# Kernel optimization log

Hardware: AMD Instinct MI355X
Metric: run time of the kernel (lower is better)

## Reference

```python
import jax, jax.numpy as jnp
import numpy as np

S = 32   # parent grid side
G = 64   # child grid side (2*S)
C = 16   # channels
DN = ('NDHWC', 'DHWIO', 'NDHWC')


def conv3(t, w, b):
    # t: [D,H,W,Cin] dense grid; zero padding == nonexistent coords contribute 0 (ME semantics)
    return jax.lax.conv_general_dilated(t[None], w, (1, 1, 1), 'SAME', dimension_numbers=DN)[0] + b


def _grids():
    ix = jnp.arange(G)
    px = (ix % 2)[:, None, None]
    py = (ix % 2)[None, :, None]
    pz = (ix % 2)[None, None, :]
    oct_m = {(a, b, c): (px == a) & (py == b) & (pz == c)
             for a in (0, 1) for b in (0, 1) for c in (0, 1)}
    groups6 = [[(0, 0, 0)], [(1, 1, 0)], [(1, 0, 1)], [(0, 1, 1)],
               [(1, 0, 0), (0, 1, 0)], [(0, 0, 1), (1, 1, 1)]]
    g6 = [jnp.any(jnp.stack([oct_m[o] for o in g]), 0) for g in groups6]
    s3 = (ix // 2)[:, None, None] + (ix // 2)[None, :, None] + (ix // 2)[None, None, :]
    m3 = [(s3 % 3) == j for j in range(3)]  # 3-way repartition (group_mask_gen_par)
    return g6, m3


def coder(feat, occ, w1, b1, w2, b2):
    # ProbCoder: conv -> ReLU -> conv -> sigmoid; outputs exist only at input coords
    of = occ[..., None].astype(feat.dtype)
    h = jax.nn.relu(conv3(feat, w1, b1)) * of
    return jax.nn.sigmoid(conv3(h, w2, b2)) * of


def union(a, b):
    (fa, oa), (fb, ob) = a, b
    return (jnp.where(oa[..., None], fa, fb), oa | ob)


def _forward(x, w_down, b_down, w_fel1, b_fel1, w_fel2, b_fel2, w_up, b_up,
             wc1, bc1, wc2, bc2, wl1, bl1, wl2, bl2):
    g6, m3 = _grids()
    occ_x = x[..., 0] > 0                                    # GT occupied child voxels
    # down (stride-2 conv): coordinate effect only -- last_POV uses ones_like features
    p_occ = jnp.any(occ_x.reshape(S, 2, S, 2, S, 2), axis=(1, 3, 5))  # parent coords
    pf = p_occ[..., None].astype(x.dtype)                    # last_POV features (ones)
    # FEL (dfa): conv(1->C,k3)+ReLU+conv(C->C,k3), outputs only at existing parents
    h = jax.nn.relu(conv3(pf, w_fel1, b_fel1)) * pf
    h = conv3(h, w_fel2, b_fel2) * pf                        # [S,S,S,C]
    # generative transposed conv k2 s2: each parent emits 8 children (octant-specific weight)
    up = jnp.einsum('xyzc,ocd->xyzod', h, w_up) + b_up       # [S,S,S,8,C]
    up = up.reshape(S, S, S, 2, 2, 2, C).transpose(0, 3, 1, 4, 2, 5, 6).reshape(G, G, G, C)
    occ = jnp.repeat(jnp.repeat(jnp.repeat(p_occ, 2, 0), 2, 1), 2, 2)  # child coords of prob
    prob_f = up * occ[..., None]
    lab = [occ_x & g for g in g6]                            # generate_label: GT per group
    # ---------- anchor1 compression (3 sub-stages inside octant group 1) ----------
    a1_o = occ & g6[0]
    a1_f = prob_f * a1_o[..., None]
    r = [(a1_f * m[..., None], a1_o & m) for m in m3]
    lab1 = [lab[0] & m for m in m3]
    p11 = coder(r[0][0], r[0][1], wc1[0], bc1[0], wc2[0], bc2[0])
    d1s = (prob_f * lab1[0][..., None], lab1[0])             # decoded GT of sub-stage 1
    in2 = union(r[1], d1s)
    p12 = coder(in2[0], in2[1], wl1[0], bl1[0], wl2[0], bl2[0]) * (in2[1] & m3[1])[..., None]
    d2s = (prob_f * lab1[1][..., None], lab1[1])
    in3 = union(union(d1s, d2s), r[2])
    p13 = coder(in3[0], in3[1], wl1[1], bl1[1], wl2[1], bl2[1]) * (in3[1] & m3[2])[..., None]
    # ---------- anchors 2..6 ----------
    dec = (prob_f * lab[0][..., None], lab[0])               # prob_anchor1_dec
    probs = [p11, p12, p13]
    for k in range(1, 6):
        ak_o = occ & g6[k]
        ak = (prob_f * ak_o[..., None], ak_o)
        inp = union(dec, ak)
        pk = coder(inp[0], inp[1], wc1[k], bc1[k], wc2[k], bc2[k]) * (inp[1] & g6[k])[..., None]
        probs.append(pk)
        if k < 5:
            dk = (prob_f * lab[k][..., None], lab[k])
            dec = union(dec, dk)
    probs = jnp.stack([p[..., 0] for p in probs], 0)          # [8,G,G,G]
    labels = jnp.stack([lab1[0], lab1[1], lab1[2], lab[1], lab[2], lab[3], lab[4], lab[5]], 0).astype(x.dtype)
    return probs, labels


def setup_inputs() -> dict:
    key = jax.random.key(0)
    ks = jax.random.split(key, 20)
    f = lambda k, s: jax.random.normal(k, s, jnp.float32) * 0.1
    x = (jax.random.uniform(ks[0], (G, G, G, 1)) < 0.5).astype(jnp.float32)
    return {
        'x': x,
        'w_down': f(ks[1], (2, 2, 2, 1, 1)), 'b_down': f(ks[2], (1,)),
        'w_fel1': f(ks[3], (3, 3, 3, 1, C)), 'b_fel1': f(ks[4], (C,)),
        'w_fel2': f(ks[5], (3, 3, 3, C, C)), 'b_fel2': f(ks[6], (C,)),
        'w_up': f(ks[7], (8, C, C)), 'b_up': f(ks[8], (C,)),
        'wc1': f(ks[9], (6, 3, 3, 3, C, C)), 'bc1': f(ks[10], (6, C)),
        'wc2': f(ks[11], (6, 3, 3, 3, C, 1)), 'bc2': f(ks[12], (6, 1)),
        'wl1': f(ks[13], (2, 5, 5, 5, C, C)), 'bl1': f(ks[14], (2, C)),
        'wl2': f(ks[15], (2, 5, 5, 5, C, 1)), 'bl2': f(ks[16], (2, 1)),
    }


def reference(x, w_down, b_down, w_fel1, b_fel1, w_fel2, b_fel2, w_up, b_up,
              wc1, bc1, wc2, bc2, wl1, bl1, wl2, bl2):
    return _forward(x, w_down, b_down, w_fel1, b_fel1, w_fel2, b_fel2, w_up, b_up,
                    wc1, bc1, wc2, bc2, wl1, bl1, wl2, bl2)
```

## Files before the change

kernel.cpp:

```cpp
#include <hip/hip_runtime.h>
#include <cstdint>
#include <math.h>

#define G 64
#define S 32
#define G3 (G*G*G)
#define S3 (S*S*S)

typedef unsigned long long u64;
typedef unsigned int u32;
typedef unsigned short u16;

typedef __attribute__((ext_vector_type(8))) short s16x8;
typedef __attribute__((ext_vector_type(4))) float f32x4;

__device__ __forceinline__ float sigmoidf_(float v) {
    return 1.0f / (1.0f + expf(-v));
}
__device__ __forceinline__ u32 f2bf_rne(float f) {
    u32 u = __float_as_uint(f);
    u += 0x7fff + ((u >> 16) & 1);
    return u >> 16;
}
__device__ __forceinline__ u64 rfl64(u64 v) {
    u32 lo = __builtin_amdgcn_readfirstlane((u32)v);
    u32 hi = __builtin_amdgcn_readfirstlane((u32)(v >> 32));
    return ((u64)hi << 32) | lo;
}
__device__ __forceinline__ u64 tap_hit(u64 wout, u64 wn, int dz) {
    return (dz >= 0) ? (wout & (wn >> dz)) : (wout & (wn << (-dz)));
}

__global__ __launch_bounds__(256) void k_pocc(const float* __restrict__ x,
                                              unsigned char* __restrict__ pocc) {
    int p = blockIdx.x * 256 + threadIdx.x;
    if (p >= S3) return;
    int pz = p & 31, py = (p >> 5) & 31, px = p >> 10;
    const float* b = x + (((size_t)(px * 2) * G + py * 2) * G + pz * 2);
    bool occ = false;
    #pragma unroll
    for (int a = 0; a < 2; a++)
        #pragma unroll
        for (int bb = 0; bb < 2; bb++)
            #pragma unroll
            for (int c = 0; c < 2; c++)
                occ = occ || (b[((size_t)a * G + bb) * G + c] > 0.0f);
    pocc[p] = occ ? 1 : 0;
}

__global__ __launch_bounds__(256) void k_fel1(const unsigned char* __restrict__ pocc,
                                              const float* __restrict__ w1,
                                              const float* __restrict__ b1,
                                              float* __restrict__ h1) {
    int p = blockIdx.x * 256 + threadIdx.x;
    if (p >= S3) return;
    int pz = p & 31, py = (p >> 5) & 31, px = p >> 10;
    float* o = h1 + (size_t)p * 16;
    if (!pocc[p]) {
        #pragma unroll
        for (int i = 0; i < 16; i++) o[i] = 0.0f;
        return;
    }
    float acc[16];
    #pragma unroll
    for (int i = 0; i < 16; i++) acc[i] = b1[i];
    for (int dx = -1; dx <= 1; ++dx) {
        int nx = px + dx; if ((unsigned)nx >= S) continue;
        for (int dy = -1; dy <= 1; ++dy) {
            int ny = py + dy; if ((unsigned)ny >= S) continue;
            for (int dz = -1; dz <= 1; ++dz) {
                int nz = pz + dz; if ((unsigned)nz >= S) continue;
                if (pocc[(nx * S + ny) * S + nz]) {
                    const float* w = w1 + (((dx + 1) * 3 + (dy + 1)) * 3 + (dz + 1)) * 16;
                    #pragma unroll
                    for (int i = 0; i < 16; i++) acc[i] += w[i];
                }
            }
        }
    }
    #pragma unroll
    for (int i = 0; i < 16; i++) o[i] = fmaxf(acc[i], 0.0f);
}

__global__ __launch_bounds__(256) void k_fel2(const unsigned char* __restrict__ pocc,
                                              const float* __restrict__ h1,
                                              const float* __restrict__ w2,
                                              const float* __restrict__ b2,
                                              float* __restrict__ h2) {
    int p = blockIdx.x * 256 + threadIdx.x;
    if (p >= S3) return;
    int pz = p & 31, py = (p >> 5) & 31, px = p >> 10;
    float* o = h2 + (size_t)p * 16;
    if (!pocc[p]) {
        #pragma unroll
        for (int i = 0; i < 16; i++) o[i] = 0.0f;
        return;
    }
    float acc[16];
    #pragma unroll
    for (int i = 0; i < 16; i++) acc[i] = b2[i];
    for (int dx = -1; dx <= 1; ++dx) {
        int nx = px + dx; if ((unsigned)nx >= S) continue;
        for (int dy = -1; dy <= 1; ++dy) {
            int ny = py + dy; if ((unsigned)ny >= S) continue;
            for (int dz = -1; dz <= 1; ++dz) {
                int nz = pz + dz; if ((unsigned)nz >= S) continue;
                const float* f = h1 + (size_t)((nx * S + ny) * S + nz) * 16;
                const float* w = w2 + (((dx + 1) * 3 + (dy + 1)) * 3 + (dz + 1)) * 256;
                #pragma unroll
                for (int ci = 0; ci < 16; ++ci) {
                    float fv = f[ci];
                    #pragma unroll
                    for (int co = 0; co < 16; ++co)
                        acc[co] = fmaf(fv, w[ci * 16 + co], acc[co]);
                }
            }
        }
    }
    #pragma unroll
    for (int i = 0; i < 16; i++) o[i] = acc[i];
}

__global__ __launch_bounds__(256) void k_up(const unsigned char* __restrict__ pocc,
                                            const float* __restrict__ h2,
                                            const float* __restrict__ wup,
                                            const float* __restrict__ bup,
                                            u16* __restrict__ probf16) {
    int p = blockIdx.x * 256 + threadIdx.x;
    if (p >= S3) return;
    int pz = p & 31, py = (p >> 5) & 31, px = p >> 10;
    bool occ = pocc[p] != 0;
    float h[16];
    const float* hp = h2 + (size_t)p * 16;
    #pragma unroll
    for (int i = 0; i < 16; i++) h[i] = hp[i];
    #pragma unroll
    for (int o = 0; o < 8; o++) {
        int a = o >> 2, b = (o >> 1) & 1, c = o & 1;
        u16* op = probf16 + (((size_t)(2 * px + a) * G + (2 * py + b)) * G + (2 * pz + c)) * 16;
        uint4* o4 = reinterpret_cast<uint4*>(op);
        if (!occ) {
            o4[0] = make_uint4(0, 0, 0, 0);
            o4[1] = make_uint4(0, 0, 0, 0);
        } else {
            u32 pk[8];
            #pragma unroll
            for (int i = 0; i < 8; ++i) {
                float a0 = bup[2 * i], a1 = bup[2 * i + 1];
                #pragma unroll
                for (int cc = 0; cc < 16; cc++) {
                    a0 = fmaf(h[cc], wup[(o * 16 + cc) * 16 + 2 * i], a0);
                    a1 = fmaf(h[cc], wup[(o * 16 + cc) * 16 + 2 * i + 1], a1);
                }
                pk[i] = f2bf_rne(a0) | (f2bf_rne(a1) << 16);
            }
            o4[0] = make_uint4(pk[0], pk[1], pk[2], pk[3]);
            o4[1] = make_uint4(pk[4], pk[5], pk[6], pk[7]);
        }
    }
}

__global__ __launch_bounds__(256) void k_masks(const float* __restrict__ x,
                                               const unsigned char* __restrict__ pocc,
                                               u64* __restrict__ lw_in,
                                               u64* __restrict__ lw_fin,
                                               float* __restrict__ labels) {
    int z = threadIdx.x;
    int y = blockIdx.x * 4 + threadIdx.y;
    int xx = blockIdx.y;
    int v = (xx * G + y) * G + z;
    int par = ((xx & 1) << 2) | ((y & 1) << 1) | (z & 1);
    const int gmap[8] = {0, 5, 4, 3, 4, 2, 1, 5};
    int g = gmap[par];
    int t = ((xx >> 1) + (y >> 1) + (z >> 1)) % 3;
    bool occ = pocc[(((xx >> 1) * S) + (y >> 1)) * S + (z >> 1)] != 0;
    bool ox = x[v] > 0.0f;
    bool g0 = (g == 0);

    bool mi[8], mf[8], lb[8];
    mi[0] = occ && g0 && (t == 0);
    mi[1] = (occ && g0 && (t == 1)) || (ox && g0 && (t == 0));
    mi[2] = (ox && g0 && (t < 2)) || (occ && g0 && (t == 2));
    mi[3] = (ox && g0)       || (occ && (g == 1));
    mi[4] = (ox && (g <= 1)) || (occ && (g == 2));
    mi[5] = (ox && (g <= 2)) || (occ && (g == 3));
    mi[6] = (ox && (g <= 3)) || (occ && (g == 4));
    mi[7] = (ox && (g <= 4)) || (occ && (g == 5));

    mf[0] = occ && g0 && (t == 0);
    mf[1] = occ && g0 && (t == 1);
    mf[2] = occ && g0 && (t == 2);
    mf[3] = occ && (g == 1);
    mf[4] = occ && (g == 2);
    mf[5] = occ && (g == 3);
    mf[6] = occ && (g == 4);
    mf[7] = occ && (g == 5);

    lb[0] = ox && g0 && (t == 0);
    lb[1] = ox && g0 && (t == 1);
    lb[2] = ox && g0 && (t == 2);
    lb[3] = ox && (g == 1);
    lb[4] = ox && (g == 2);
    lb[5] = ox && (g == 3);
    lb[6] = ox && (g == 4);
    lb[7] = ox && (g == 5);

    int line = xx * G + y;
    #pragma unroll
    for (int c = 0; c < 8; ++c) {
        u64 wi = __ballot((int)mi[c]);
        u64 wf = __ballot((int)mf[c]);
        if (z == 0) {
            lw_in[c * 4096 + line] = wi;
            lw_fin[c * 4096 + line] = wf;
        }
        labels[(size_t)c * G3 + v] = lb[c] ? 1.0f : 0.0f;
    }
}

#define FRAGSTRIDE 38400
__global__ __launch_bounds__(64) void k_prep_bfrag(const float* __restrict__ wc1,
                                                   const float* __restrict__ wl1,
                                                   u16* __restrict__ bfrag) {
    int c = blockIdx.x;
    int frag = blockIdx.y;
    int lane = threadIdx.x;
    bool is5 = (c == 1 || c == 2);
    int R = is5 ? 2 : 1;
    int KS = 2 * R + 1;
    int npair = R + 1;
    int nfrag = KS * KS * npair;
    if (frag >= nfrag) return;
    const float* W = is5 ? (wl1 + (size_t)(c - 1) * 32000)
                         : (wc1 + (size_t)((c == 0) ? 0 : (c - 2)) * 6912);
    int dxdy = frag / npair, p = frag - dxdy * npair;
    int dxi = dxdy / KS, dyi = dxdy - dxi * KS;
    int dziA = 2 * p, dziB = 2 * p + 1;
    int co = lane & 15, kg = lane >> 4;
    u16 outv[8];
    #pragma unroll
    for (int j = 0; j < 8; ++j) {
        int k = kg * 8 + j;
        int ci = k & 15;
        int dzi = (k < 16) ? dziA : dziB;
        float v = 0.0f;
        if (dzi < KS)
            v = W[(size_t)((dxi * KS + dyi) * KS + dzi) * 256 + ci * 16 + co];
        outv[j] = (u16)f2bf_rne(v);
    }
    u16* o = bfrag + (size_t)c * FRAGSTRIDE + ((size_t)frag * 64 + lane) * 8;
    uint4 pk;
    pk.x = outv[0] | ((u32)outv[1] << 16);
    pk.y = outv[2] | ((u32)outv[3] << 16);
    pk.z = outv[4] | ((u32)outv[5] << 16);
    pk.w = outv[6] | ((u32)outv[7] << 16);
    *reinterpret_cast<uint4*>(o) = pk;
}

__global__ __launch_bounds__(256) void k_conv1_mfma(const u16* __restrict__ probf16,
                                                    const u64* __restrict__ lw_in,
                                                    const u16* __restrict__ bfrag,
                                                    const float* __restrict__ bc1,
                                                    const float* __restrict__ bl1,
                                                    u16* __restrict__ hbase,
                                                    int coderBase) {
    int c = coderBase + blockIdx.y;
    bool is5 = (c == 1 || c == 2);
    int R = is5 ? 2 : 1;
    int KS = 2 * R + 1, npair = R + 1;
    const u64* lw = lw_in + (size_t)c * 4096;
    u16* h_c = hbase + (size_t)blockIdx.y * G3 * 16;
    const u16* bf = bfrag + (size_t)c * FRAGSTRIDE;
    const float* bptr = is5 ? (bl1 + (c - 1) * 16)
                            : (bc1 + ((c == 0) ? 0 : (c - 2)) * 16);

    int x = blockIdx.x >> 4;
    int y0 = (blockIdx.x & 15) << 2;
    int w = threadIdx.y;
    int lane = threadIdx.x;
    int yw = y0 + w;

    u64 w0 = rfl64(lw[x * G + yw]);
    u64 anyw = lw[x * G + y0] | lw[x * G + y0 + 1] | lw[x * G + y0 + 2] | lw[x * G + y0 + 3];
    if (anyw == 0ULL) return;

    __shared__ u32 lds[8 * 2304 / 4];

    int col = lane & 15, kg = lane >> 4;
    float bv = bptr[col];
    f32x4 acc[4];
    #pragma unroll
    for (int s = 0; s < 4; ++s) acc[s] = (f32x4){bv, bv, bv, bv};

    int nlines = 4 + 2 * R;
    int nunits = nlines * 144;
    int t = w * 64 + lane;

    for (int dx = -R; dx <= R; ++dx) {
        int nx = x + dx;
        __syncthreads();
        if ((unsigned)nx < G) {
            for (int u = t; u < nunits; u += 256) {
                int s = u / 144; int q = u - s * 144;
                int lz = q >> 1, half = q & 1;
                int gz = lz - 4;
                int ny = y0 - R + s;
                uint4 val = make_uint4(0, 0, 0, 0);
                if ((unsigned)ny < G && (unsigned)gz < G) {
                    u64 wn = lw[nx * G + ny];
                    if ((wn >> gz) & 1)
                        val = *reinterpret_cast<const uint4*>(
                            probf16 + ((size_t)((nx * G + ny) * G + gz) * 16 + half * 8));
                }
                *reinterpret_cast<uint4*>(
                    reinterpret_cast<char*>(lds) + s * 2304 + half * 1152 + lz * 16) = val;
            }
        }
        __syncthreads();
        if (w0 == 0ULL || (unsigned)nx >= G) continue;

        for (int dy = -R; dy <= R; ++dy) {
            int ny = yw + dy;
            if ((unsigned)ny >= G) continue;
            u64 wn = rfl64(lw[nx * G + ny]);
            if (wn == 0ULL) continue;
            int slot = w + dy + R;
            for (int p = 0; p < npair; ++p) {
                int dzA = -R + 2 * p;
                int dzB = dzA + 1;
                bool hasB = (dzB <= R);
                u64 hit = tap_hit(w0, wn, dzA);
                if (hasB) hit |= tap_hit(w0, wn, dzB);
                if (hit == 0ULL) continue;
                int frag = ((dx + R) * KS + (dy + R)) * npair + p;
                s16x8 bf8 = *reinterpret_cast<const s16x8*>(bf + ((size_t)frag * 64 + lane) * 8);
                int dz = (kg < 2) ? dzA : (hasB ? dzB : dzA);
                int lzb = (lane & 15) + dz + 4;
                const char* abase = reinterpret_cast<const char*>(lds)
                                    + slot * 2304 + (kg & 1) * 1152;
                #pragma unroll
                for (int s = 0; s < 4; ++s) {
                    if (((hit >> (s * 16)) & 0xFFFFULL) == 0ULL) continue;
                    s16x8 a = *reinterpret_cast<const s16x8*>(abase + (s * 16 + lzb) * 16);
                    acc[s] = __builtin_amdgcn_mfma_f32_16x16x32_bf16(a, bf8, acc[s], 0, 0, 0);
                }
            }
        }
    }

    if (w0 == 0ULL) return;
    u16* hline = h_c + (size_t)(x * G + yw) * G * 16;
    #pragma unroll
    for (int s = 0; s < 4; ++s) {
        #pragma unroll
        for (int r = 0; r < 4; ++r) {
            int z = s * 16 + kg * 4 + r;
            if ((w0 >> z) & 1) {
                float v = fmaxf(acc[s][r], 0.0f);
                hline[z * 16 + col] = (u16)f2bf_rne(v);
            }
        }
    }
}

template <int KS>
__device__ __forceinline__ void conv2_body(const u32* __restrict__ h_c,
                                           const u64* __restrict__ lwi,
                                           const u64* __restrict__ lwf,
                                           const float* __restrict__ w2,
                                           const float* __restrict__ b2,
                                           float* __restrict__ outp) {
    const int R = KS / 2;
    int z = threadIdx.x;
    int line = blockIdx.x * 4 + threadIdx.y;
    int xx = line >> 6, y = line & 63;
    int v = (xx * G + y) * G + z;
    u64 wf = rfl64(lwf[line]);
    if (wf == 0ULL) { outp[v] = 0.0f; return; }
    bool m = (wf >> z) & 1;

    float acc = b2[0];
    for (int dx = -R; dx <= R; ++dx) {
        int nx = xx + dx; if ((unsigned)nx >= G) continue;
        for (int dy = -R; dy <= R; ++dy) {
            int ny = y + dy; if ((unsigned)ny >= G) continue;
            u64 wn = rfl64(lwi[nx * G + ny]);
            if (wn == 0ULL) continue;
            const float* wbase = w2 + (size_t)(((dx + R) * KS + (dy + R)) * KS) * 16;
            #pragma unroll
            for (int dz = -R; dz <= R; ++dz) {
                if (tap_hit(wf, wn, dz) == 0ULL) continue;
                int nz = z + dz;
                bool ok = (unsigned)nz < G;
                int nzc = ok ? nz : 0;
                bool mn = ok && ((wn >> nzc) & 1);
                const float* w = wbase + (dz + R) * 16;
                if (mn) {
                    const uint4* h4 = reinterpret_cast<const uint4*>(
                        h_c + ((size_t)((nx * G + ny) * G + nzc)) * 8);
                    uint4 Ua = h4[0], Ub = h4[1];
                    u32 uu[8] = {Ua.x, Ua.y, Ua.z, Ua.w, Ub.x, Ub.y, Ub.z, Ub.w};
                    #pragma unroll
                    for (int i = 0; i < 8; ++i) {
                        float lo = __uint_as_float(uu[i] << 16);
                        float hi = __uint_as_float(uu[i] & 0xffff0000u);
                        acc = fmaf(lo, w[2 * i], acc);
                        acc = fmaf(hi, w[2 * i + 1], acc);
                    }
                }
            }
        }
    }
    outp[v] = m ? sigmoidf_(acc) : 0.0f;
}

__global__ __launch_bounds__(256) void k_conv2_all(const u32* __restrict__ hbase,
                                                   const u64* __restrict__ lw_in,
                                                   const u64* __restrict__ lw_fin,
                                                   const float* __restrict__ wc2,
                                                   const float* __restrict__ bc2,
                                                   const float* __restrict__ wl2,
                                                   const float* __restrict__ bl2,
                                                   float* __restrict__ out,
                                                   int coderBase) {
    int c = coderBase + blockIdx.y;
    const u64* lwi = lw_in + (size_t)c * 4096;
    const u64* lwf = lw_fin + (size_t)c * 4096;
    const u32* h_c = hbase + (size_t)blockIdx.y * G3 * 8;
    float* outp = out + (size_t)c * G3;
    if (c == 1 || c == 2) {
        conv2_body<5>(h_c, lwi, lwf, wl2 + (size_t)(c - 1) * 2000, bl2 + (c - 1), outp);
    } else {
        int j = (c == 0) ? 0 : (c - 2);
        conv2_body<3>(h_c, lwi, lwf, wc2 + (size_t)j * 432, bc2 + j, outp);
    }
}

extern "C" void kernel_launch(void* const* d_in, const int* in_sizes, int n_in,
                              void* d_out, int out_size, void* d_ws, size_t ws_size,
                              hipStream_t stream) {
    const float* x      = (const float*)d_in[0];
    const float* w_fel1 = (const float*)d_in[3];
    const float* b_fel1 = (const float*)d_in[4];
    const float* w_fel2 = (const float*)d_in[5];
    const float* b_fel2 = (const float*)d_in[6];
    const float* w_up   = (const float*)d_in[7];
    const float* b_up   = (const float*)d_in[8];
    const float* wc1    = (const float*)d_in[9];
    const float* bc1    = (const float*)d_in[10];
    const float* wc2    = (const float*)d_in[11];
    const float* bc2    = (const float*)d_in[12];
    const float* wl1    = (const float*)d_in[13];
    const float* bl1    = (const float*)d_in[14];
    const float* wl2    = (const float*)d_in[15];
    const float* bl2    = (const float*)d_in[16];
    float* out = (float*)d_out;

    char* ws = (char*)d_ws;
    u16*  probf16 = (u16*)(ws);
    float* h1     = (float*)(ws + 8388608);
    float* h2     = (float*)(ws + 10485760);
    unsigned char* pocc = (unsigned char*)(ws + 12582912);
    u64* lw_in  = (u64*)(ws + 12615680);
    u64* lw_fin = (u64*)(ws + 12877824);
    u16* bfrag  = (u16*)(ws + 13139968);
    u16* hbase  = (u16*)(ws + 13754368);

    const size_t fixed_end = 13754368;
    const size_t hsz = (size_t)G3 * 16 * 2;
    int B = 2;
    if (fixed_end + 8 * hsz <= ws_size) B = 8;
    else if (fixed_end + 4 * hsz <= ws_size) B = 4;

    k_pocc <<<dim3(S3 / 256), dim3(256), 0, stream>>>(x, pocc);
    k_fel1 <<<dim3(S3 / 256), dim3(256), 0, stream>>>(pocc, w_fel1, b_fel1, h1);
    k_fel2 <<<dim3(S3 / 256), dim3(256), 0, stream>>>(pocc, h1, w_fel2, b_fel2, h2);
    k_up   <<<dim3(S3 / 256), dim3(256), 0, stream>>>(pocc, h2, w_up, b_up, probf16);
    k_masks<<<dim3(16, 64), dim3(64, 4), 0, stream>>>(x, pocc, lw_in, lw_fin, out + (size_t)8 * G3);
    k_prep_bfrag<<<dim3(8, 75), dim3(64), 0, stream>>>(wc1, wl1, bfrag);

    for (int b0 = 0; b0 < 8; b0 += B) {
        int nb = (8 - b0 < B) ? (8 - b0) : B;
        k_conv1_mfma<<<dim3(1024, nb), dim3(64, 4), 0, stream>>>(
            probf16, lw_in, bfrag, bc1, bl1, hbase, b0);
        k_conv2_all<<<dim3(1024, nb), dim3(64, 4), 0, stream>>>(
            (const u32*)hbase, lw_in, lw_fin, wc2, bc2, wl2, bl2, out, b0);
    }
}
```

Baseline: 212.1 us.

## Swizzle conv1 LDS layout, split conv2 accumulators, launch all coders at once

The conv1 LDS staging buffer moves from a split-half layout to an interleaved 32-byte-per-z layout with an XOR swizzle on the half index, meant to cut bank conflicts on MFMA A-operand reads. conv2 now accumulates into two independent partial sums to shorten the dependent FMA chain. The batched coder loop is removed, and both conv kernels launch once over all 8 coders, which assumes the workspace can hold 8 hidden buffers. There are also small index simplifications in the bfrag prep kernel.

New measurement: 213.3 us, median of 2. No clear change (+0.5%).

```diff
diff --git a/kernel.cpp b/kernel.cpp
--- a/kernel.cpp
+++ b/kernel.cpp
@@ -125,7 +125,7 @@
                                             const float* __restrict__ h2,
                                             const float* __restrict__ wup,
                                             const float* __restrict__ bup,
-                                            u16* __restrict__ probf16) {
+                                            u16* __restrict__ pf) {
     int p = blockIdx.x * 256 + threadIdx.x;
     if (p >= S3) return;
     int pz = p & 31, py = (p >> 5) & 31, px = p >> 10;
@@ -137,7 +137,7 @@
     #pragma unroll
     for (int o = 0; o < 8; o++) {
         int a = o >> 2, b = (o >> 1) & 1, c = o & 1;
-        u16* op = probf16 + (((size_t)(2 * px + a) * G + (2 * py + b)) * G + (2 * pz + c)) * 16;
+        u16* op = pf + (((size_t)(2 * px + a) * G + (2 * py + b)) * G + (2 * pz + c)) * 16;
         uint4* o4 = reinterpret_cast<uint4*>(op);
         if (!occ) {
             o4[0] = make_uint4(0, 0, 0, 0);
@@ -234,18 +234,17 @@
     const float* W = is5 ? (wl1 + (size_t)(c - 1) * 32000)
                          : (wc1 + (size_t)((c == 0) ? 0 : (c - 2)) * 6912);
     int dxdy = frag / npair, p = frag - dxdy * npair;
-    int dxi = dxdy / KS, dyi = dxdy - dxi * KS;
-    int dziA = 2 * p, dziB = 2 * p + 1;
+    int dziA = 2 * p;
     int co = lane & 15, kg = lane >> 4;
     u16 outv[8];
     #pragma unroll
     for (int j = 0; j < 8; ++j) {
         int k = kg * 8 + j;
         int ci = k & 15;
-        int dzi = (k < 16) ? dziA : dziB;
+        int dzi = (k < 16) ? dziA : (dziA + 1);
         float v = 0.0f;
         if (dzi < KS)
-            v = W[(size_t)((dxi * KS + dyi) * KS + dzi) * 256 + ci * 16 + co];
+            v = W[(size_t)(dxdy * KS + dzi) * 256 + ci * 16 + co];
         outv[j] = (u16)f2bf_rne(v);
     }
     u16* o = bfrag + (size_t)c * FRAGSTRIDE + ((size_t)frag * 64 + lane) * 8;
@@ -257,19 +256,18 @@
     *reinterpret_cast<uint4*>(o) = pk;
 }
 
-__global__ __launch_bounds__(256) void k_conv1_mfma(const u16* __restrict__ probf16,
+__global__ __launch_bounds__(256) void k_conv1_mfma(const u16* __restrict__ pf,
                                                     const u64* __restrict__ lw_in,
                                                     const u16* __restrict__ bfrag,
                                                     const float* __restrict__ bc1,
                                                     const float* __restrict__ bl1,
-                                                    u16* __restrict__ hbase,
-                                                    int coderBase) {
-    int c = coderBase + blockIdx.y;
+                                                    u16* __restrict__ hbase) {
+    int c = blockIdx.y;
     bool is5 = (c == 1 || c == 2);
     int R = is5 ? 2 : 1;
     int KS = 2 * R + 1, npair = R + 1;
     const u64* lw = lw_in + (size_t)c * 4096;
-    u16* h_c = hbase + (size_t)blockIdx.y * G3 * 16;
+    u16* h_c = hbase + (size_t)c * G3 * 16;
     const u16* bf = bfrag + (size_t)c * FRAGSTRIDE;
     const float* bptr = is5 ? (bl1 + (c - 1) * 16)
                             : (bc1 + ((c == 0) ? 0 : (c - 2)) * 16);
@@ -310,10 +308,11 @@
                     u64 wn = lw[nx * G + ny];
                     if ((wn >> gz) & 1)
                         val = *reinterpret_cast<const uint4*>(
-                            probf16 + ((size_t)((nx * G + ny) * G + gz) * 16 + half * 8));
+                            pf + ((size_t)((nx * G + ny) * G + gz) * 16 + half * 8));
                 }
                 *reinterpret_cast<uint4*>(
-                    reinterpret_cast<char*>(lds) + s * 2304 + half * 1152 + lz * 16) = val;
+                    reinterpret_cast<char*>(lds) + s * 2304 + lz * 32 +
+                    ((half ^ ((lz >> 2) & 1)) * 16)) = val;
             }
         }
         __syncthreads();
@@ -335,13 +334,14 @@
                 int frag = ((dx + R) * KS + (dy + R)) * npair + p;
                 s16x8 bf8 = *reinterpret_cast<const s16x8*>(bf + ((size_t)frag * 64 + lane) * 8);
                 int dz = (kg < 2) ? dzA : (hasB ? dzB : dzA);
-                int lzb = (lane & 15) + dz + 4;
-                const char* abase = reinterpret_cast<const char*>(lds)
-                                    + slot * 2304 + (kg & 1) * 1152;
+                int lzb = col + dz + 4;
+                const char* ab = reinterpret_cast<const char*>(lds)
+                                 + slot * 2304 + lzb * 32
+                                 + (((kg & 1) ^ ((lzb >> 2) & 1)) * 16);
                 #pragma unroll
                 for (int s = 0; s < 4; ++s) {
                     if (((hit >> (s * 16)) & 0xFFFFULL) == 0ULL) continue;
-                    s16x8 a = *reinterpret_cast<const s16x8*>(abase + (s * 16 + lzb) * 16);
+                    s16x8 a = *reinterpret_cast<const s16x8*>(ab + s * 512);
                     acc[s] = __builtin_amdgcn_mfma_f32_16x16x32_bf16(a, bf8, acc[s], 0, 0, 0);
                 }
             }
@@ -379,7 +379,7 @@
     if (wf == 0ULL) { outp[v] = 0.0f; return; }
     bool m = (wf >> z) & 1;
 
-    float acc = b2[0];
+    float ac0 = 0.0f, ac1 = 0.0f;
     for (int dx = -R; dx <= R; ++dx) {
         int nx = xx + dx; if ((unsigned)nx >= G) continue;
         for (int dy = -R; dy <= R; ++dy) {
@@ -400,17 +400,21 @@
                         h_c + ((size_t)((nx * G + ny) * G + nzc)) * 8);
                     uint4 Ua = h4[0], Ub = h4[1];
                     u32 uu[8] = {Ua.x, Ua.y, Ua.z, Ua.w, Ub.x, Ub.y, Ub.z, Ub.w};
+                    float s0 = 0.0f, s1 = 0.0f;
                     #pragma unroll
                     for (int i = 0; i < 8; ++i) {
                         float lo = __uint_as_float(uu[i] << 16);
                         float hi = __uint_as_float(uu[i] & 0xffff0000u);
-                        acc = fmaf(lo, w[2 * i], acc);
-                        acc = fmaf(hi, w[2 * i + 1], acc);
+                        s0 = fmaf(lo, w[2 * i], s0);
+                        s1 = fmaf(hi, w[2 * i + 1], s1);
                     }
-                }
-            }
-        }
-    }
+                    if (((dz + R) & 1) == 0) ac0 += s0 + s1;
+                    else                     ac1 += s0 + s1;
+                }
+            }
+        }
+    }
+    float acc = b2[0] + ac0 + ac1;
     outp[v] = m ? sigmoidf_(acc) : 0.0f;
 }
 
@@ -421,12 +425,11 @@
                                                    const float* __restrict__ bc2,
                                                    const float* __restrict__ wl2,
                                                    const float* __restrict__ bl2,
-                                                   float* __restrict__ out,
-                                                   int coderBase) {
-    int c = coderBase + blockIdx.y;
+                                                   float* __restrict__ out) {
+    int c = blockIdx.y;
     const u64* lwi = lw_in + (size_t)c * 4096;
     const u64* lwf = lw_fin + (size_t)c * 4096;
-    const u32* h_c = hbase + (size_t)blockIdx.y * G3 * 8;
+    const u32* h_c = hbase + (size_t)c * G3 * 8;
     float* outp = out + (size_t)c * G3;
     if (c == 1 || c == 2) {
         conv2_body<5>(h_c, lwi, lwf, wl2 + (size_t)(c - 1) * 2000, bl2 + (c - 1), outp);
@@ -466,12 +469,6 @@
     u16* bfrag  = (u16*)(ws + 13139968);
     u16* hbase  = (u16*)(ws + 13754368);
 
-    const size_t fixed_end = 13754368;
-    const size_t hsz = (size_t)G3 * 16 * 2;
-    int B = 2;
-    if (fixed_end + 8 * hsz <= ws_size) B = 8;
-    else if (fixed_end + 4 * hsz <= ws_size) B = 4;
-
     k_pocc <<<dim3(S3 / 256), dim3(256), 0, stream>>>(x, pocc);
     k_fel1 <<<dim3(S3 / 256), dim3(256), 0, stream>>>(pocc, w_fel1, b_fel1, h1);
     k_fel2 <<<dim3(S3 / 256), dim3(256), 0, stream>>>(pocc, h1, w_fel2, b_fel2, h2);
@@ -479,11 +476,8 @@
     k_masks<<<dim3(16, 64), dim3(64, 4), 0, stream>>>(x, pocc, lw_in, lw_fin, out + (size_t)8 * G3);
     k_prep_bfrag<<<dim3(8, 75), dim3(64), 0, stream>>>(wc1, wl1, bfrag);
 
-    for (int b0 = 0; b0 < 8; b0 += B) {
-        int nb = (8 - b0 < B) ? (8 - b0) : B;
-        k_conv1_mfma<<<dim3(1024, nb), dim3(64, 4), 0, stream>>>(
-            probf16, lw_in, bfrag, bc1, bl1, hbase, b0);
-        k_conv2_all<<<dim3(1024, nb), dim3(64, 4), 0, stream>>>(
-            (const u32*)hbase, lw_in, lw_fin, wc2, bc2, wl2, bl2, out, b0);
-    }
-}
+    k_conv1_mfma<<<dim3(1024, 8), dim3(64, 4), 0, stream>>>(
+        probf16, lw_in, bfrag, bc1, bl1, hbase);
+    k_conv2_all<<<dim3(1024, 8), dim3(64, 4), 0, stream>>>(
+        (const u32*)hbase, lw_in, lw_fin, wc2, bc2, wl2, bl2, out);
+}
```
